# Kernel optimization log

Measured on AMD Instinct MI355X. Metric: run time of the kernel, lower is better.

Reference implementation:

```python
import jax, jax.numpy as jnp
import numpy as np

B, C, IMG, P, D, L, NH, DFF = 8, 2, 256, 16, 1024, 8, 16, 4096
HP = IMG // P          # 16 patches per side
N = HP * HP            # 256 patch tokens
S = N + 1              # + cls token
HD = D // NH           # 64 head dim


def _ln(x, w, b, eps=1e-5):
    mu = x.mean(-1, keepdims=True)
    var = ((x - mu) ** 2).mean(-1, keepdims=True)
    return (x - mu) * jax.lax.rsqrt(var + eps) * w + b


def _decay_mask():
    # RetNetRelPos2d(D, NH, initial_value=1, heads_range=NH): per-head log-decay
    decay = jnp.log(1.0 - 2.0 ** (-1.0 - NH * jnp.arange(NH, dtype=jnp.float32) / NH))
    idx = jnp.arange(HP)
    gy, gx = jnp.meshgrid(idx, idx, indexing='ij')
    grid = jnp.stack([gy.ravel(), gx.ravel()], -1)                 # [N,2]
    dist = jnp.abs(grid[:, None] - grid[None, :]).sum(-1)          # [N,N] Manhattan
    mask = decay[:, None, None] * dist.astype(jnp.float32)        # [NH,N,N]
    return jnp.pad(mask, ((0, 0), (1, 0), (1, 0)))                 # cls: zero decay


def setup_inputs() -> dict:
    key = jax.random.key(0)
    ks = iter(jax.random.split(key, 16))
    g = lambda shape: jax.random.normal(next(ks), shape, jnp.float32) * 0.02
    return dict(
        imgs=jax.random.normal(next(ks), (B, C, IMG, IMG), jnp.float32),
        patch_w=g((C, P, P, D)), patch_b=jnp.zeros((D,), jnp.float32),
        cls_tok=g((1, 1, D)),
        ln1_w=jnp.ones((L, D), jnp.float32), ln1_b=jnp.zeros((L, D), jnp.float32),
        wq=g((L, D, D)), wk=g((L, D, D)), wv=g((L, D, D)),
        bq=jnp.zeros((L, D), jnp.float32), bk=jnp.zeros((L, D), jnp.float32), bv=jnp.zeros((L, D), jnp.float32),
        wo=g((L, D, D)), bo=jnp.zeros((L, D), jnp.float32),
        ln2_w=jnp.ones((L, D), jnp.float32), ln2_b=jnp.zeros((L, D), jnp.float32),
        w1=g((L, D, DFF)), b1=jnp.zeros((L, DFF), jnp.float32),
        w2=g((L, DFF, D)), b2=jnp.zeros((L, D), jnp.float32),
        normf_w=jnp.ones((D,), jnp.float32), normf_b=jnp.zeros((D,), jnp.float32),
        enpred_w=g((D, P * P * 2)), enpred_b=jnp.zeros((P * P * 2,), jnp.float32),
    )


def reference(imgs, patch_w, patch_b, cls_tok, ln1_w, ln1_b, wq, wk, wv, bq, bk, bv,
              wo, bo, ln2_w, ln2_b, w1, b1, w2, b2, normf_w, normf_b, enpred_w, enpred_b):
    b = imgs.shape[0]
    # PatchEmbed: conv with stride==kernel == patch extraction + linear
    xp = imgs.reshape(b, C, HP, P, HP, P)
    x = jnp.einsum('nchpwq,cpqd->nhwd', xp, patch_w).reshape(b, N, D) + patch_b
    residual = x
    x = jnp.concatenate([jnp.broadcast_to(cls_tok, (b, 1, D)), x], axis=1)  # [b,S,D]
    mask = _decay_mask()  # [NH,S,S]
    scale = HD ** -0.5
    for i in range(L):  # RMT blocks: pre-LN MaSA (softmax(qk*scale + decay)) + pre-LN GELU MLP
        h = _ln(x, ln1_w[i], ln1_b[i])
        q = (h @ wq[i] + bq[i]).reshape(b, S, NH, HD)
        k = (h @ wk[i] + bk[i]).reshape(b, S, NH, HD)
        v = (h @ wv[i] + bv[i]).reshape(b, S, NH, HD)
        logits = jnp.einsum('bqhd,bkhd->bhqk', q, k) * scale + mask
        attn = jax.nn.softmax(logits, axis=-1)
        o = jnp.einsum('bhqk,bkhd->bqhd', attn, v).reshape(b, S, D)
        x = x + o @ wo[i] + bo[i]
        h = _ln(x, ln2_w[i], ln2_b[i])
        x = x + jax.nn.gelu(h @ w1[i] + b1[i], approximate=False) @ w2[i] + b2[i]
    x = _ln(x, normf_w, normf_b)
    # PGSA on patch tokens as [b,D,HP,HP]
    t = x[:, 1:, :].transpose(0, 2, 1).reshape(b, D, HP, HP)
    n = HP * HP - 1
    mu = t.mean(axis=(2, 3), keepdims=True)
    xm2 = (t - mu) ** 2
    y = xm2 / (4.0 * (xm2.sum(axis=(2, 3), keepdims=True) / n + 1e-4)) + 0.5
    t = t * jax.nn.sigmoid(y)
    tokens = t.reshape(b, D, N).transpose(0, 2, 1) + residual
    pred = tokens @ enpred_w + enpred_b  # [b,N,P*P*2]
    # unpatchify -> [b,2,IMG,IMG]
    u = pred.reshape(b, HP, HP, P, P, 2)
    return jnp.einsum('nhwpqc->nchpwq', u).reshape(b, 2, IMG, IMG)
```

## Files before the change

kernel.cpp:

```cpp
#include <hip/hip_runtime.h>
#include <cstdint>
#include <cstddef>

#define BB    8
#define CCH   2
#define IMGD  256
#define PDIM  16
#define DD    1024
#define LLAY  8
#define NHEAD 16
#define DFFD  4096
#define NTOK  256
#define SD    257
#define HDD   64
#define MTOK  (BB*SD)
#define MPAT  (BB*NTOK)
#define MPAD  2176
#define KPAD  288
#define QSTR  3072

typedef unsigned short u16;
typedef __bf16 bf16x8 __attribute__((ext_vector_type(8)));
typedef float  f32x4  __attribute__((ext_vector_type(4)));

__device__ __forceinline__ u16 f2bf(float f) {
    uint32_t u = __float_as_uint(f);
    u += 0x7FFF + ((u >> 16) & 1);
    return (u16)(u >> 16);
}
__device__ __forceinline__ int imin(int a, int b) { return a < b ? a : b; }

#define GLB(p)  ((const __attribute__((address_space(1))) void*)(uintptr_t)(p))
#define LDSP(p) ((__attribute__((address_space(3))) void*)(uint32_t)(uintptr_t)(p))

__device__ __forceinline__ void tp64(const float* __restrict__ W,
                                     u16* __restrict__ WT, int K, int N,
                                     int k0, int n0, float (*t)[65])
{
    const int c = threadIdx.x & 63, r4 = threadIdx.x >> 6;
    #pragma unroll
    for (int i = 0; i < 16; ++i) {
        const int r = i * 4 + r4;
        t[r][c] = W[(size_t)(k0 + r) * N + n0 + c];
    }
    __syncthreads();
    #pragma unroll
    for (int i = 0; i < 16; ++i) {
        const int r = i * 4 + r4;
        WT[(size_t)(n0 + r) * K + k0 + c] = f2bf(t[c][r]);
    }
}

__device__ __forceinline__ void tp_dispatch(
    int t, const float* wqN, const float* wkN, const float* wvN,
    const float* woN, const float* w1N, const float* w2N,
    u16* WTqkvN, u16* WTwoN, u16* WTw1N, u16* WTw2N, float (*tb)[65])
{
    if (t < 768) {
        const int which = t >> 8, local = t & 255;
        const float* W = which == 0 ? wqN : which == 1 ? wkN : wvN;
        tp64(W, WTqkvN + (size_t)which * 1024 * DD, DD, DD,
             (local >> 4) * 64, (local & 15) * 64, tb);
    } else if (t < 1024) {
        const int local = t - 768;
        tp64(woN, WTwoN, DD, DD, (local >> 4) * 64, (local & 15) * 64, tb);
    } else if (t < 2048) {
        const int local = t - 1024;
        tp64(w1N, WTw1N, DD, DFFD, (local >> 6) * 64, (local & 63) * 64, tb);
    } else {
        const int local = t - 2048;
        tp64(w2N, WTw2N, DFFD, DD, (local >> 4) * 64, (local & 15) * 64, tb);
    }
}

__global__ __launch_bounds__(256) void mlp1_tp(
    const u16* __restrict__ A, const u16* __restrict__ BT,
    const float* __restrict__ bias, u16* __restrict__ Cout, int M,
    const float* __restrict__ wqN, const float* __restrict__ wkN,
    const float* __restrict__ wvN, const float* __restrict__ woN,
    const float* __restrict__ w1N, const float* __restrict__ w2N,
    u16* __restrict__ WTqkvN, u16* __restrict__ WTwoN,
    u16* __restrict__ WTw1N, u16* __restrict__ WTw2N)
{
    __shared__ float smem[64 * 65];
    if (blockIdx.y >= 17) {
        const int t = (blockIdx.y - 17) * 32 + blockIdx.x;
        tp_dispatch(t, wqN, wkN, wvN, woN, w1N, w2N,
                    WTqkvN, WTwoN, WTw1N, WTw2N, (float(*)[65])smem);
        return;
    }
    u16* lds = (u16*)smem;
    const int N = DFFD, K = DD;
    const int tid = threadIdx.x, wid = tid >> 6, lane = tid & 63;
    const int m0 = blockIdx.y * 128, n0 = blockIdx.x * 128;
    const int wm = (wid >> 1) * 64, wn = (wid & 1) * 64;
    const int srow = lane >> 2, scol = (lane & 3) * 8;
    const int l15 = lane & 15, loct = lane >> 4;

    f32x4 acc[4][4] = {};
    const size_t arow = (size_t)(m0 + wid * 16 + srow) * K + scol;
    const size_t brow = (size_t)(n0 + wid * 16 + srow) * K + scol;
    u16* ldsA = lds + wid * 512;
    u16* ldsB = lds + 4096 + wid * 512;

    for (int k0 = 0; k0 < K; k0 += 32) {
        __builtin_amdgcn_global_load_lds(GLB(A  + arow + k0),                 LDSP(ldsA),        16, 0, 0);
        __builtin_amdgcn_global_load_lds(GLB(A  + arow + (size_t)64*K + k0),  LDSP(ldsA + 2048), 16, 0, 0);
        __builtin_amdgcn_global_load_lds(GLB(BT + brow + k0),                 LDSP(ldsB),        16, 0, 0);
        __builtin_amdgcn_global_load_lds(GLB(BT + brow + (size_t)64*K + k0),  LDSP(ldsB + 2048), 16, 0, 0);
        __syncthreads();
        bf16x8 af[4], bfr[4];
        #pragma unroll
        for (int i = 0; i < 4; ++i)
            af[i] = *(const bf16x8*)(lds + (wm + i * 16 + l15) * 32 + loct * 8);
        #pragma unroll
        for (int j = 0; j < 4; ++j)
            bfr[j] = *(const bf16x8*)(lds + 4096 + (wn + j * 16 + l15) * 32 + loct * 8);
        #pragma unroll
        for (int i = 0; i < 4; ++i)
            #pragma unroll
            for (int j = 0; j < 4; ++j)
                acc[i][j] = __builtin_amdgcn_mfma_f32_16x16x32_bf16(af[i], bfr[j], acc[i][j], 0, 0, 0);
        __syncthreads();
    }

    #pragma unroll
    for (int j = 0; j < 4; ++j) {
        const int col = n0 + wn + j * 16 + l15;
        const float bv = bias[col];
        #pragma unroll
        for (int i = 0; i < 4; ++i) {
            const int rbase = m0 + wm + i * 16 + loct * 4;
            #pragma unroll
            for (int r = 0; r < 4; ++r) {
                const int row = rbase + r;
                if (row < M) {
                    float v = acc[i][j][r] + bv;
                    v = 0.5f * v * (1.f + erff(v * 0.70710678118654752f));
                    Cout[(size_t)row * N + col] = f2bf(v);
                }
            }
        }
    }
}

template<int SPLIT>
__global__ __launch_bounds__(256) void gemm128_skp(
    const u16* __restrict__ A, const u16* __restrict__ BT,
    float* __restrict__ P, int M, int N, int K)
{
    __shared__ u16 lds[8192];
    const int tid = threadIdx.x, wid = tid >> 6, lane = tid & 63;
    const int m0 = blockIdx.y * 128, n0 = blockIdx.x * 128;
    const int wm = (wid >> 1) * 64, wn = (wid & 1) * 64;
    const int srow = lane >> 2, scol = (lane & 3) * 8;
    const int l15 = lane & 15, loct = lane >> 4;
    const int Ks = K / SPLIT;
    const int kb = blockIdx.z * Ks;

    f32x4 acc[4][4] = {};
    const size_t arow = (size_t)(m0 + wid * 16 + srow) * K + scol + kb;
    const size_t brow = (size_t)(n0 + wid * 16 + srow) * K + scol + kb;
    u16* ldsA = lds + wid * 512;
    u16* ldsB = lds + 4096 + wid * 512;

    for (int k0 = 0; k0 < Ks; k0 += 32) {
        __builtin_amdgcn_global_load_lds(GLB(A  + arow + k0),                 LDSP(ldsA),        16, 0, 0);
        __builtin_amdgcn_global_load_lds(GLB(A  + arow + (size_t)64*K + k0),  LDSP(ldsA + 2048), 16, 0, 0);
        __builtin_amdgcn_global_load_lds(GLB(BT + brow + k0),                 LDSP(ldsB),        16, 0, 0);
        __builtin_amdgcn_global_load_lds(GLB(BT + brow + (size_t)64*K + k0),  LDSP(ldsB + 2048), 16, 0, 0);
        __syncthreads();
        bf16x8 af[4], bfr[4];
        #pragma unroll
        for (int i = 0; i < 4; ++i)
            af[i] = *(const bf16x8*)(lds + (wm + i * 16 + l15) * 32 + loct * 8);
        #pragma unroll
        for (int j = 0; j < 4; ++j)
            bfr[j] = *(const bf16x8*)(lds + 4096 + (wn + j * 16 + l15) * 32 + loct * 8);
        #pragma unroll
        for (int i = 0; i < 4; ++i)
            #pragma unroll
            for (int j = 0; j < 4; ++j)
                acc[i][j] = __builtin_amdgcn_mfma_f32_16x16x32_bf16(af[i], bfr[j], acc[i][j], 0, 0, 0);
        __syncthreads();
    }

    float* Pz = P + (size_t)blockIdx.z * M * N;
    #pragma unroll
    for (int j = 0; j < 4; ++j) {
        const int col = n0 + wn + j * 16 + l15;
        #pragma unroll
        for (int i = 0; i < 4; ++i) {
            const int rbase = m0 + wm + i * 16 + loct * 4;
            #pragma unroll
            for (int r = 0; r < 4; ++r) {
                const int row = rbase + r;
                if (row < M) Pz[(size_t)row * N + col] = acc[i][j][r];
            }
        }
    }
}

__global__ __launch_bounds__(256) void gemm_qkv(
    const u16* __restrict__ A, const u16* __restrict__ BT,
    const float* __restrict__ bq, const float* __restrict__ bk,
    const float* __restrict__ bvp,
    u16* __restrict__ QKVb, int M, int K)
{
    __shared__ u16 lds[8192];
    const int tid = threadIdx.x, wid = tid >> 6, lane = tid & 63;
    const int m0 = blockIdx.y * 128, n0 = blockIdx.x * 128;
    const int wm = (wid >> 1) * 64, wn = (wid & 1) * 64;
    const int srow = lane >> 2, scol = (lane & 3) * 8;
    const int l15 = lane & 15, loct = lane >> 4;

    f32x4 acc[4][4] = {};
    const size_t arow = (size_t)(m0 + wid * 16 + srow) * K + scol;
    const size_t brow = (size_t)(n0 + wid * 16 + srow) * K + scol;
    u16* ldsA = lds + wid * 512;
    u16* ldsB = lds + 4096 + wid * 512;

    for (int k0 = 0; k0 < K; k0 += 32) {
        __builtin_amdgcn_global_load_lds(GLB(A  + arow + k0),                 LDSP(ldsA),        16, 0, 0);
        __builtin_amdgcn_global_load_lds(GLB(A  + arow + (size_t)64*K + k0),  LDSP(ldsA + 2048), 16, 0, 0);
        __builtin_amdgcn_global_load_lds(GLB(BT + brow + k0),                 LDSP(ldsB),        16, 0, 0);
        __builtin_amdgcn_global_load_lds(GLB(BT + brow + (size_t)64*K + k0),  LDSP(ldsB + 2048), 16, 0, 0);
        __syncthreads();
        bf16x8 af[4], bfr[4];
        #pragma unroll
        for (int i = 0; i < 4; ++i)
            af[i] = *(const bf16x8*)(lds + (wm + i * 16 + l15) * 32 + loct * 8);
        #pragma unroll
        for (int j = 0; j < 4; ++j)
            bfr[j] = *(const bf16x8*)(lds + 4096 + (wn + j * 16 + l15) * 32 + loct * 8);
        #pragma unroll
        for (int i = 0; i < 4; ++i)
            #pragma unroll
            for (int j = 0; j < 4; ++j)
                acc[i][j] = __builtin_amdgcn_mfma_f32_16x16x32_bf16(af[i], bfr[j], acc[i][j], 0, 0, 0);
        __syncthreads();
    }

    #pragma unroll
    for (int j = 0; j < 4; ++j) {
        const int col = n0 + wn + j * 16 + l15;
        const float bval = (col < 1024) ? bq[col]
                         : (col < 2048) ? bk[col - 1024]
                                        : bvp[col - 2048];
        #pragma unroll
        for (int i = 0; i < 4; ++i) {
            const int rbase = m0 + wm + i * 16 + loct * 4;
            #pragma unroll
            for (int r = 0; r < 4; ++r) {
                const int row = rbase + r;
                if (row < M)
                    QKVb[(size_t)row * QSTR + col] = f2bf(acc[i][j][r] + bval);
            }
        }
    }
}

__global__ __launch_bounds__(256) void vt_k(const u16* __restrict__ QKVb,
                                            u16* __restrict__ VTg)
{
    __shared__ u16 t[64][66];
    const int h0 = blockIdx.x * 64, k0 = blockIdx.y * 64, b = blockIdx.z;
    const int c = threadIdx.x & 63, r4 = threadIdx.x >> 6;
    #pragma unroll
    for (int i = 0; i < 16; ++i) {
        const int key = k0 + i * 4 + r4;
        t[i * 4 + r4][c] = (key < SD)
            ? QKVb[((size_t)(b * SD + key)) * QSTR + 2048 + h0 + c] : (u16)0;
    }
    __syncthreads();
    const int key = k0 + c;
    if (key < KPAD) {
        #pragma unroll
        for (int i = 0; i < 16; ++i) {
            const int hd = i * 4 + r4;
            VTg[((size_t)(b * 1024 + h0 + hd)) * KPAD + key] = t[c][hd];
        }
    }
}

__global__ __launch_bounds__(256) void patch_tp(
    const u16* __restrict__ A, const u16* __restrict__ BT,
    const float* __restrict__ bias, float* __restrict__ Cout,
    const float* __restrict__ wq0, const float* __restrict__ wk0,
    const float* __restrict__ wv0, const float* __restrict__ wo0,
    const float* __restrict__ w10, const float* __restrict__ w20,
    u16* __restrict__ WTqkv0, u16* __restrict__ WTwo0,
    u16* __restrict__ WTw10, u16* __restrict__ WTw20)
{
    __shared__ float smem[64 * 65];
    if (blockIdx.y >= 32) {
        const int t = (blockIdx.y - 32) * 16 + blockIdx.x;
        tp_dispatch(t, wq0, wk0, wv0, wo0, w10, w20,
                    WTqkv0, WTwo0, WTw10, WTw20, (float(*)[65])smem);
        return;
    }
    u16* lds = (u16*)smem;
    const int N = DD, K = 512;
    const int tid = threadIdx.x, wid = tid >> 6, lane = tid & 63;
    const int m0 = blockIdx.y * 64, n0 = blockIdx.x * 64;
    const int wm = (wid >> 1) * 32, wn = (wid & 1) * 32;
    const int srow = lane >> 2, scol = (lane & 3) * 8;
    const int l15 = lane & 15, loct = lane >> 4;

    f32x4 acc[2][2] = {};
    const size_t arow = (size_t)(m0 + wid * 16 + srow) * K + scol;
    const size_t brow = (size_t)(n0 + wid * 16 + srow) * K + scol;
    u16* ldsA = lds + wid * 512;
    u16* ldsB = lds + 4096 + wid * 512;

    for (int k0 = 0; k0 < K; k0 += 64) {
        __builtin_amdgcn_global_load_lds(GLB(A  + arow + k0),      LDSP(ldsA),        16, 0, 0);
        __builtin_amdgcn_global_load_lds(GLB(A  + arow + k0 + 32), LDSP(ldsA + 2048), 16, 0, 0);
        __builtin_amdgcn_global_load_lds(GLB(BT + brow + k0),      LDSP(ldsB),        16, 0, 0);
        __builtin_amdgcn_global_load_lds(GLB(BT + brow + k0 + 32), LDSP(ldsB + 2048), 16, 0, 0);
        __syncthreads();
        #pragma unroll
        for (int t = 0; t < 2; ++t) {
            bf16x8 af[2], bfr[2];
            #pragma unroll
            for (int i = 0; i < 2; ++i)
                af[i] = *(const bf16x8*)(lds + t * 2048 + (wm + i * 16 + l15) * 32 + loct * 8);
            #pragma unroll
            for (int j = 0; j < 2; ++j)
                bfr[j] = *(const bf16x8*)(lds + 4096 + t * 2048 + (wn + j * 16 + l15) * 32 + loct * 8);
            #pragma unroll
            for (int i = 0; i < 2; ++i)
                #pragma unroll
                for (int j = 0; j < 2; ++j)
                    acc[i][j] = __builtin_amdgcn_mfma_f32_16x16x32_bf16(af[i], bfr[j], acc[i][j], 0, 0, 0);
        }
        __syncthreads();
    }

    #pragma unroll
    for (int j = 0; j < 2; ++j) {
        const int col = n0 + wn + j * 16 + l15;
        const float bv = bias[col];
        #pragma unroll
        for (int i = 0; i < 2; ++i) {
            const int rbase = m0 + wm + i * 16 + loct * 4;
            #pragma unroll
            for (int r = 0; r < 4; ++r) {
                const int row = rbase + r;
                Cout[(size_t)row * N + col] = acc[i][j][r] + bv;
            }
        }
    }
}

template<int ACT, int OBF>
__global__ __launch_bounds__(256) void gemm64(
    const u16* __restrict__ A, const u16* __restrict__ BT,
    const float* __restrict__ bias, const float* __restrict__ Cin,
    void* __restrict__ Cout, int M, int N, int K)
{
    __shared__ u16 lds[8192];
    const int tid = threadIdx.x, wid = tid >> 6, lane = tid & 63;
    const int m0 = blockIdx.y * 64, n0 = blockIdx.x * 64;
    const int wm = (wid >> 1) * 32, wn = (wid & 1) * 32;
    const int srow = lane >> 2, scol = (lane & 3) * 8;
    const int l15 = lane & 15, loct = lane >> 4;

    f32x4 acc[2][2] = {};
    const size_t arow = (size_t)(m0 + wid * 16 + srow) * K + scol;
    const size_t brow = (size_t)(n0 + wid * 16 + srow) * K + scol;
    u16* ldsA = lds + wid * 512;
    u16* ldsB = lds + 4096 + wid * 512;

    for (int k0 = 0; k0 < K; k0 += 64) {
        __builtin_amdgcn_global_load_lds(GLB(A  + arow + k0),      LDSP(ldsA),        16, 0, 0);
        __builtin_amdgcn_global_load_lds(GLB(A  + arow + k0 + 32), LDSP(ldsA + 2048), 16, 0, 0);
        __builtin_amdgcn_global_load_lds(GLB(BT + brow + k0),      LDSP(ldsB),        16, 0, 0);
        __builtin_amdgcn_global_load_lds(GLB(BT + brow + k0 + 32), LDSP(ldsB + 2048), 16, 0, 0);
        __syncthreads();
        #pragma unroll
        for (int t = 0; t < 2; ++t) {
            bf16x8 af[2], bfr[2];
            #pragma unroll
            for (int i = 0; i < 2; ++i)
                af[i] = *(const bf16x8*)(lds + t * 2048 + (wm + i * 16 + l15) * 32 + loct * 8);
            #pragma unroll
            for (int j = 0; j < 2; ++j)
                bfr[j] = *(const bf16x8*)(lds + 4096 + t * 2048 + (wn + j * 16 + l15) * 32 + loct * 8);
            #pragma unroll
            for (int i = 0; i < 2; ++i)
                #pragma unroll
                for (int j = 0; j < 2; ++j)
                    acc[i][j] = __builtin_amdgcn_mfma_f32_16x16x32_bf16(af[i], bfr[j], acc[i][j], 0, 0, 0);
        }
        __syncthreads();
    }

    #pragma unroll
    for (int j = 0; j < 2; ++j) {
        const int col = n0 + wn + j * 16 + l15;
        const float bv = bias[col];
        #pragma unroll
        for (int i = 0; i < 2; ++i) {
            const int rbase = m0 + wm + i * 16 + loct * 4;
            #pragma unroll
            for (int r = 0; r < 4; ++r) {
                const int row = rbase + r;
                if (row < M) {
                    float v = acc[i][j][r] + bv;
                    if (ACT) v = 0.5f * v * (1.f + erff(v * 0.70710678118654752f));
                    if (Cin) v += Cin[(size_t)row * N + col];
                    if (OBF) ((u16*)Cout)[(size_t)row * N + col] = f2bf(v);
                    else     ((float*)Cout)[(size_t)row * N + col] = v;
                }
            }
        }
    }
}

__global__ __launch_bounds__(256) void attn_fused(
    const u16* __restrict__ QKVb, const u16* __restrict__ VTg,
    u16* __restrict__ O)
{
    __shared__ u16 P[4][16][296];
    const int tid = threadIdx.x, wid = tid >> 6, lane = tid & 63;
    const int l15 = lane & 15, loct = lane >> 4;
    const int bh = blockIdx.x, b = bh >> 4, h = bh & 15;
    const int q0 = blockIdx.y * 64 + wid * 16;

    const size_t qkbase = (size_t)b * SD * QSTR + h * 64;
    const u16* qp = QKVb + qkbase + (size_t)imin(q0 + l15, SD - 1) * QSTR;
    const bf16x8 qf0 = *(const bf16x8*)(qp + loct * 8);
    const bf16x8 qf1 = *(const bf16x8*)(qp + 32 + loct * 8);

    f32x4 s[17];
    #pragma unroll
    for (int nt = 0; nt < 17; ++nt) {
        const u16* kp = QKVb + qkbase + (size_t)imin(nt * 16 + l15, SD - 1) * QSTR + 1024;
        const bf16x8 kf0 = *(const bf16x8*)(kp + loct * 8);
        const bf16x8 kf1 = *(const bf16x8*)(kp + 32 + loct * 8);
        f32x4 a = {};
        a = __builtin_amdgcn_mfma_f32_16x16x32_bf16(qf0, kf0, a, 0, 0, 0);
        a = __builtin_amdgcn_mfma_f32_16x16x32_bf16(qf1, kf1, a, 0, 0, 0);
        s[nt] = a;
    }

    const float dec = logf(1.f - exp2f(-1.f - (float)h));
    const int qb = q0 + loct * 4;
    float rmax[4] = {-3.4e38f, -3.4e38f, -3.4e38f, -3.4e38f};
    #pragma unroll
    for (int nt = 0; nt < 17; ++nt) {
        const int key = nt * 16 + l15;
        #pragma unroll
        for (int r = 0; r < 4; ++r) {
            float v;
            if (key >= SD) {
                v = -1e30f;
            } else {
                v = s[nt][r] * 0.125f;
                const int q = qb + r;
                if (q > 0 && key > 0) {
                    const int nq = q - 1, nk = key - 1;
                    const int dist = abs((nq >> 4) - (nk >> 4)) + abs((nq & 15) - (nk & 15));
                    v += dec * (float)dist;
                }
            }
            s[nt][r] = v;
            rmax[r] = fmaxf(rmax[r], v);
        }
    }
    #pragma unroll
    for (int r = 0; r < 4; ++r) {
        #pragma unroll
        for (int m = 1; m < 16; m <<= 1) rmax[r] = fmaxf(rmax[r], __shfl_xor(rmax[r], m));
    }
    float rsum[4] = {0.f, 0.f, 0.f, 0.f};
    #pragma unroll
    for (int nt = 0; nt < 17; ++nt)
        #pragma unroll
        for (int r = 0; r < 4; ++r) {
            const float e = __expf(s[nt][r] - rmax[r]);
            s[nt][r] = e;
            rsum[r] += e;
        }
    #pragma unroll
    for (int r = 0; r < 4; ++r) {
        #pragma unroll
        for (int m = 1; m < 16; m <<= 1) rsum[r] += __shfl_xor(rsum[r], m);
        rsum[r] = 1.f / rsum[r];
    }
    #pragma unroll
    for (int nt = 0; nt < 17; ++nt)
        #pragma unroll
        for (int r = 0; r < 4; ++r)
            P[wid][loct * 4 + r][nt * 16 + l15] = f2bf(s[nt][r] * rsum[r]);
    {
        const int rr = lane >> 2, cc = (lane & 3) * 4;
        #pragma unroll
        for (int i = 0; i < 4; ++i) P[wid][rr][272 + cc + i] = 0;
    }

    f32x4 o[4] = {};
    const u16* vrow = VTg + ((size_t)b * 1024 + h * 64) * KPAD;
    #pragma unroll
    for (int ks = 0; ks < 9; ++ks) {
        const bf16x8 pf = *(const bf16x8*)&P[wid][l15][ks * 32 + loct * 8];
        #pragma unroll
        for (int j = 0; j < 4; ++j) {
            const bf16x8 vf = *(const bf16x8*)(vrow + (size_t)(j * 16 + l15) * KPAD + ks * 32 + loct * 8);
            o[j] = __builtin_amdgcn_mfma_f32_16x16x32_bf16(pf, vf, o[j], 0, 0, 0);
        }
    }
    #pragma unroll
    for (int j = 0; j < 4; ++j)
        #pragma unroll
        for (int r = 0; r < 4; ++r) {
            const int q = qb + r;
            if (q < SD) O[((size_t)(b * SD + q)) * DD + h * 64 + j * 16 + l15] = f2bf(o[j][r]);
        }
}

__global__ __launch_bounds__(256) void transpose_bf16_b(
    const float* __restrict__ W, u16* __restrict__ WT, int K, int N,
    size_t sstrideZ, size_t dstrideZ)
{
    __shared__ float t[64][65];
    tp64(W + (size_t)blockIdx.z * sstrideZ, WT + (size_t)blockIdx.z * dstrideZ,
         K, N, blockIdx.y * 64, blockIdx.x * 64, t);
}

__global__ __launch_bounds__(256) void im2col_k(const float* __restrict__ imgs,
                                                u16* __restrict__ Ao)
{
    const int idx = blockIdx.x * 256 + threadIdx.x;
    const int k = idx & 511, m = idx >> 9;
    const int b = m >> 8, n = m & 255;
    const int hp = n >> 4, wp = n & 15;
    const int c = k >> 8, p = (k >> 4) & 15, q = k & 15;
    Ao[idx] = f2bf(imgs[(((size_t)b * CCH + c) * IMGD + hp * PDIM + p) * IMGD + wp * PDIM + q]);
}

__global__ __launch_bounds__(256) void build_x_k(const float* __restrict__ RES,
                                                 const float* __restrict__ cls,
                                                 float* __restrict__ X)
{
    const int idx = blockIdx.x * 256 + threadIdx.x;
    const int d = idx & 1023;
    const int r = idx >> 10;
    const int b = r / SD;
    const int s = r - b * SD;
    X[idx] = (s == 0) ? cls[d] : RES[((size_t)(b * NTOK + s - 1)) * DD + d];
}

template<int NP, int OBF>
__global__ __launch_bounds__(256) void ln_rows_c(
    float* __restrict__ X, const float* __restrict__ PB, size_t pstride,
    const float* __restrict__ badd,
    const float* __restrict__ w, const float* __restrict__ bsrc,
    void* __restrict__ Y)
{
    const int wid = threadIdx.x >> 6, lane = threadIdx.x & 63;
    const int row = blockIdx.x * 4 + wid;
    float* xr = X + (size_t)row * DD;
    float4 v[4];
    float s = 0.f, s2 = 0.f;
    #pragma unroll
    for (int i = 0; i < 4; ++i) {
        const int cc = (i * 64 + lane) * 4;
        v[i] = *(const float4*)(xr + cc);
        if (NP) {
            const float4 bb = *(const float4*)(badd + cc);
            v[i].x += bb.x; v[i].y += bb.y; v[i].z += bb.z; v[i].w += bb.w;
            #pragma unroll
            for (int p = 0; p < NP; ++p) {
                const float4 pv = *(const float4*)(PB + (size_t)p * pstride + (size_t)row * DD + cc);
                v[i].x += pv.x; v[i].y += pv.y; v[i].z += pv.z; v[i].w += pv.w;
            }
            *(float4*)(xr + cc) = v[i];
        }
        s  += v[i].x + v[i].y + v[i].z + v[i].w;
        s2 += v[i].x * v[i].x + v[i].y * v[i].y + v[i].z * v[i].z + v[i].w * v[i].w;
    }
    #pragma unroll
    for (int off = 1; off < 64; off <<= 1) {
        s  += __shfl_xor(s, off);
        s2 += __shfl_xor(s2, off);
    }
    const float mu  = s * (1.f / 1024.f);
    const float var = fmaf(-mu, mu, s2 * (1.f / 1024.f));
    const float ri  = rsqrtf(var + 1e-5f);
    #pragma unroll
    for (int i = 0; i < 4; ++i) {
        const int cc = (i * 64 + lane) * 4;
        const float4 wv = *(const float4*)(w + cc);
        const float4 bv = *(const float4*)(bsrc + cc);
        float4 o;
        o.x = (v[i].x - mu) * ri * wv.x + bv.x;
        o.y = (v[i].y - mu) * ri * wv.y + bv.y;
        o.z = (v[i].z - mu) * ri * wv.z + bv.z;
        o.w = (v[i].w - mu) * ri * wv.w + bv.w;
        if (OBF) {
            ushort4 o4 = make_ushort4(f2bf(o.x), f2bf(o.y), f2bf(o.z), f2bf(o.w));
            *(ushort4*)((u16*)Y + (size_t)row * DD + cc) = o4;
        } else {
            *(float4*)((float*)Y + (size_t)row * DD + cc) = o;
        }
    }
}

__global__ __launch_bounds__(256) void pgsa_k(const float* __restrict__ Xf,
                                              const float* __restrict__ RES,
                                              u16* __restrict__ TOK)
{
    const int bd = blockIdx.x;
    const int b = bd >> 10, dch = bd & 1023;
    const int n = threadIdx.x;
    const float t = Xf[((size_t)(b * SD + 1 + n)) * DD + dch];
    __shared__ float red[4];
    float s = t;
    #pragma unroll
    for (int off = 1; off < 64; off <<= 1) s += __shfl_xor(s, off);
    if ((n & 63) == 0) red[n >> 6] = s;
    __syncthreads();
    const float mu = (red[0] + red[1] + red[2] + red[3]) * (1.f / 256.f);
    const float xm = t - mu;
    const float xm2 = xm * xm;
    __syncthreads();
    float s2 = xm2;
    #pragma unroll
    for (int off = 1; off < 64; off <<= 1) s2 += __shfl_xor(s2, off);
    if ((n & 63) == 0) red[n >> 6] = s2;
    __syncthreads();
    const float tot2 = red[0] + red[1] + red[2] + red[3];
    const float y = xm2 / (4.f * (tot2 * (1.f / 255.f) + 1e-4f)) + 0.5f;
    const float sig = 1.f / (1.f + expf(-y));
    const size_t ri = ((size_t)b * NTOK + n) * DD + dch;
    TOK[ri] = f2bf(fmaf(t, sig, RES[ri]));
}

__global__ __launch_bounds__(256) void unpatch_k(const float* __restrict__ PRED,
                                                 float* __restrict__ out)
{
    const int idx = blockIdx.x * 256 + threadIdx.x;
    const int j = idx & 255, i = (idx >> 8) & 255;
    const int c = (idx >> 16) & 1, b = idx >> 17;
    const int hp = i >> 4, p = i & 15, wp = j >> 4, q = j & 15;
    out[idx] = PRED[((size_t)b * NTOK + hp * 16 + wp) * 512 + (p * 16 + q) * 2 + c];
}

extern "C" void kernel_launch(void* const* d_in, const int* in_sizes, int n_in,
                              void* d_out, int out_size, void* d_ws, size_t ws_size,
                              hipStream_t stream)
{
    const float* imgs     = (const float*)d_in[0];
    const float* patch_w  = (const float*)d_in[1];
    const float* patch_b  = (const float*)d_in[2];
    const float* cls_tok  = (const float*)d_in[3];
    const float* ln1_w    = (const float*)d_in[4];
    const float* ln1_b    = (const float*)d_in[5];
    const float* wq       = (const float*)d_in[6];
    const float* wk       = (const float*)d_in[7];
    const float* wv       = (const float*)d_in[8];
    const float* bq       = (const float*)d_in[9];
    const float* bk       = (const float*)d_in[10];
    const float* bv       = (const float*)d_in[11];
    const float* wo       = (const float*)d_in[12];
    const float* bo       = (const float*)d_in[13];
    const float* ln2_w    = (const float*)d_in[14];
    const float* ln2_b    = (const float*)d_in[15];
    const float* w1       = (const float*)d_in[16];
    const float* b1       = (const float*)d_in[17];
    const float* w2       = (const float*)d_in[18];
    const float* b2       = (const float*)d_in[19];
    const float* normf_w  = (const float*)d_in[20];
    const float* normf_b  = (const float*)d_in[21];
    const float* enpred_w = (const float*)d_in[22];
    const float* enpred_b = (const float*)d_in[23];
    float* out = (float*)d_out;

    char* w = (char*)d_ws;
    float* X     = (float*)w;            w += (size_t)MTOK * DD * 4;
    float* RES   = (float*)w;            w += (size_t)MPAT * DD * 4;
    u16*   QKVb  = (u16*)w;              w += (size_t)MPAD * QSTR * 2;
    u16*   VTg   = (u16*)w;              w += (size_t)BB * 1024 * KPAD * 2;
    char*  UNION = w;                    w += (size_t)MPAD * DFFD * 2;
    u16*   Hb    = (u16*)w;              w += (size_t)MPAD * DD * 2;
    u16*   Ob    = (u16*)w;              w += (size_t)MPAD * DD * 2;
    float* PART  = (float*)w;            w += (size_t)4 * MTOK * DD * 4;
    u16*   WTqkv = (u16*)w;              w += (size_t)LLAY * 3072 * DD * 2;
    u16*   WTwo  = (u16*)w;              w += (size_t)LLAY * DD * DD * 2;
    u16*   WTw1  = (u16*)w;              w += (size_t)LLAY * DFFD * DD * 2;
    u16*   WTw2  = (u16*)w;              w += (size_t)LLAY * DD * DFFD * 2;
    u16*   WTpe  = (u16*)w;              w += (size_t)DD * 512 * 2;
    u16*   WTen  = (u16*)w;              w += (size_t)512 * DD * 2;

    u16*   IM2b  = (u16*)UNION;
    u16*   GELUb = (u16*)UNION;
    float* PRED  = (float*)UNION;
    float* Hf    = (float*)QKVb;
    u16*   TOKb  = Hb;
    const size_t PSTR = (size_t)MTOK * DD;

    hipLaunchKernelGGL(transpose_bf16_b, dim3(DD / 64, 512 / 64, 1), dim3(256), 0, stream,
                       patch_w, WTpe, 512, DD, (size_t)0, (size_t)0);
    hipLaunchKernelGGL(transpose_bf16_b, dim3(512 / 64, DD / 64, 1), dim3(256), 0, stream,
                       enpred_w, WTen, DD, 512, (size_t)0, (size_t)0);
    hipLaunchKernelGGL(im2col_k, dim3(4096), dim3(256), 0, stream, imgs, IM2b);

    hipLaunchKernelGGL(patch_tp, dim3(DD / 64, 32 + 192), dim3(256), 0, stream,
                       IM2b, WTpe, patch_b, RES,
                       wq, wk, wv, wo, w1, w2,
                       WTqkv, WTwo, WTw1, WTw2);
    hipLaunchKernelGGL(build_x_k, dim3(MTOK * DD / 256), dim3(256), 0, stream, RES, cls_tok, X);

    for (int i = 0; i < LLAY; ++i) {
        if (i == 0)
            hipLaunchKernelGGL((ln_rows_c<0,1>), dim3(MTOK / 4), dim3(256), 0, stream,
                               X, (const float*)nullptr, (size_t)0, (const float*)nullptr,
                               ln1_w + i * DD, ln1_b + i * DD, (void*)Hb);
        else
            hipLaunchKernelGGL((ln_rows_c<4,1>), dim3(MTOK / 4), dim3(256), 0, stream,
                               X, PART, PSTR, b2 + (i - 1) * DD,
                               ln1_w + i * DD, ln1_b + i * DD, (void*)Hb);
        hipLaunchKernelGGL(gemm_qkv, dim3(3072 / 128, 17), dim3(256), 0, stream,
                           Hb, WTqkv + (size_t)i * 3072 * DD,
                           bq + i * DD, bk + i * DD, bv + i * DD, QKVb, MTOK, DD);
        hipLaunchKernelGGL(vt_k, dim3(16, 5, BB), dim3(256), 0, stream, QKVb, VTg);
        hipLaunchKernelGGL(attn_fused, dim3(BB * NHEAD, 5), dim3(256), 0, stream,
                           QKVb, VTg, Ob);
        hipLaunchKernelGGL((gemm64<0,0>), dim3(DD / 64, 33), dim3(256), 0, stream,
                           Ob, WTwo + (size_t)i * DD * DD, bo + i * DD, X, (void*)X, MTOK, DD, DD);
        hipLaunchKernelGGL((ln_rows_c<0,1>), dim3(MTOK / 4), dim3(256), 0, stream,
                           X, (const float*)nullptr, (size_t)0, (const float*)nullptr,
                           ln2_w + i * DD, ln2_b + i * DD, (void*)Hb);
        if (i < LLAY - 1) {
            const size_t n1 = (size_t)(i + 1);
            hipLaunchKernelGGL(mlp1_tp, dim3(DFFD / 128, 17 + 96), dim3(256), 0, stream,
                               Hb, WTw1 + (size_t)i * DFFD * DD, b1 + i * DFFD, GELUb, MTOK,
                               wq + n1 * DD * DD, wk + n1 * DD * DD, wv + n1 * DD * DD,
                               wo + n1 * DD * DD, w1 + n1 * DD * DFFD, w2 + n1 * DFFD * DD,
                               WTqkv + n1 * 3072 * DD, WTwo + n1 * DD * DD,
                               WTw1 + n1 * DFFD * DD, WTw2 + n1 * DD * DFFD);
        } else {
            hipLaunchKernelGGL(mlp1_tp, dim3(DFFD / 128, 17), dim3(256), 0, stream,
                               Hb, WTw1 + (size_t)i * DFFD * DD, b1 + i * DFFD, GELUb, MTOK,
                               (const float*)nullptr, (const float*)nullptr, (const float*)nullptr,
                               (const float*)nullptr, (const float*)nullptr, (const float*)nullptr,
                               (u16*)nullptr, (u16*)nullptr, (u16*)nullptr, (u16*)nullptr);
        }
        hipLaunchKernelGGL((gemm128_skp<4>), dim3(DD / 128, 17, 4), dim3(256), 0, stream,
                           GELUb, WTw2 + (size_t)i * DD * DFFD, PART, MTOK, DD, DFFD);
    }

    hipLaunchKernelGGL((ln_rows_c<4,0>), dim3(MTOK / 4), dim3(256), 0, stream,
                       X, PART, PSTR, b2 + (LLAY - 1) * DD, normf_w, normf_b, (void*)Hf);
    hipLaunchKernelGGL(pgsa_k, dim3(BB * DD), dim3(256), 0, stream, Hf, RES, TOKb);
    hipLaunchKernelGGL((gemm64<0,0>), dim3(512 / 64, MPAT / 64), dim3(256), 0, stream,
                       TOKb, WTen, enpred_b, (const float*)nullptr, (void*)PRED, MPAT, 512, DD);
    hipLaunchKernelGGL(unpatch_k, dim3(4096), dim3(256), 0, stream, PRED, out);
}
```

Baseline: 1.925 ms.

## Fuse V transpose into QKV GEMM epilogue, restructure PGSA and unpatchify

The QKV GEMM now writes Q and K into a narrower 2048-column buffer and scatters V directly into the transposed VTg layout through LDS. This removes the separate vt_k kernel and its round trip through global memory, and VTg is zeroed once with a memset so the key padding stays valid. PGSA switches to coalesced per-channel column processing that computes sum and sum of squares in one pass, and unpatchify reads float2 pairs and writes both channels. The scattered, strided VTg writes in the epilogue may be poorly coalesced, and the one-pass variance formula changes numerics slightly.

Result: faster. 1.858 ms (-3.5%).

```diff
diff --git a/kernel.cpp b/kernel.cpp
--- a/kernel.cpp
+++ b/kernel.cpp
@@ -17,7 +17,6 @@
 #define MPAT  (BB*NTOK)
 #define MPAD  2176
 #define KPAD  288
-#define QSTR  3072
 
 typedef unsigned short u16;
 typedef __bf16 bf16x8 __attribute__((ext_vector_type(8)));
@@ -205,9 +204,9 @@
     const u16* __restrict__ A, const u16* __restrict__ BT,
     const float* __restrict__ bq, const float* __restrict__ bk,
     const float* __restrict__ bvp,
-    u16* __restrict__ QKVb, int M, int K)
-{
-    __shared__ u16 lds[8192];
+    u16* __restrict__ QKb, u16* __restrict__ VTg, int M, int K)
+{
+    __shared__ u16 lds[128 * 66];
     const int tid = threadIdx.x, wid = tid >> 6, lane = tid & 63;
     const int m0 = blockIdx.y * 128, n0 = blockIdx.x * 128;
     const int wm = (wid >> 1) * 64, wn = (wid & 1) * 64;
@@ -241,44 +240,57 @@
         __syncthreads();
     }
 
-    #pragma unroll
-    for (int j = 0; j < 4; ++j) {
-        const int col = n0 + wn + j * 16 + l15;
-        const float bval = (col < 1024) ? bq[col]
-                         : (col < 2048) ? bk[col - 1024]
-                                        : bvp[col - 2048];
-        #pragma unroll
-        for (int i = 0; i < 4; ++i) {
-            const int rbase = m0 + wm + i * 16 + loct * 4;
-            #pragma unroll
-            for (int r = 0; r < 4; ++r) {
-                const int row = rbase + r;
-                if (row < M)
-                    QKVb[(size_t)row * QSTR + col] = f2bf(acc[i][j][r] + bval);
-            }
-        }
-    }
-}
-
-__global__ __launch_bounds__(256) void vt_k(const u16* __restrict__ QKVb,
-                                            u16* __restrict__ VTg)
-{
-    __shared__ u16 t[64][66];
-    const int h0 = blockIdx.x * 64, k0 = blockIdx.y * 64, b = blockIdx.z;
-    const int c = threadIdx.x & 63, r4 = threadIdx.x >> 6;
-    #pragma unroll
-    for (int i = 0; i < 16; ++i) {
-        const int key = k0 + i * 4 + r4;
-        t[i * 4 + r4][c] = (key < SD)
-            ? QKVb[((size_t)(b * SD + key)) * QSTR + 2048 + h0 + c] : (u16)0;
-    }
-    __syncthreads();
-    const int key = k0 + c;
-    if (key < KPAD) {
-        #pragma unroll
-        for (int i = 0; i < 16; ++i) {
-            const int hd = i * 4 + r4;
-            VTg[((size_t)(b * 1024 + h0 + hd)) * KPAD + key] = t[c][hd];
+    if (n0 < 2048) {
+        #pragma unroll
+        for (int j = 0; j < 4; ++j) {
+            const int col = n0 + wn + j * 16 + l15;
+            const float bval = (col < 1024) ? bq[col] : bk[col - 1024];
+            #pragma unroll
+            for (int i = 0; i < 4; ++i) {
+                const int rbase = m0 + wm + i * 16 + loct * 4;
+                #pragma unroll
+                for (int r = 0; r < 4; ++r) {
+                    const int row = rbase + r;
+                    if (row < M)
+                        QKb[(size_t)row * 2048 + col] = f2bf(acc[i][j][r] + bval);
+                }
+            }
+        }
+    } else {
+        const int hd0 = n0 - 2048;
+        #pragma unroll
+        for (int h = 0; h < 2; ++h) {
+            __syncthreads();
+            if ((wn >> 6) == h) {
+                #pragma unroll
+                for (int j = 0; j < 4; ++j) {
+                    const int c = j * 16 + l15;
+                    const float bval = bvp[hd0 + h * 64 + c];
+                    #pragma unroll
+                    for (int i = 0; i < 4; ++i) {
+                        const int rbase = wm + i * 16 + loct * 4;
+                        #pragma unroll
+                        for (int r = 0; r < 4; ++r)
+                            lds[(rbase + r) * 66 + c] = f2bf(acc[i][j][r] + bval);
+                    }
+                }
+            }
+            __syncthreads();
+            const int rowLane = tid & 63, cIdx = tid >> 6;
+            #pragma unroll
+            for (int cc = 0; cc < 16; ++cc) {
+                const int c = cIdx * 16 + cc;
+                #pragma unroll
+                for (int rh = 0; rh < 2; ++rh) {
+                    const int row = rowLane + rh * 64;
+                    const int g = m0 + row;
+                    if (g < M) {
+                        const int b = g / SD, key = g - b * SD;
+                        VTg[((size_t)b * 1024 + hd0 + h * 64 + c) * KPAD + key] =
+                            lds[row * 66 + c];
+                    }
+                }
+            }
         }
     }
 }
@@ -419,7 +431,7 @@
 }
 
 __global__ __launch_bounds__(256) void attn_fused(
-    const u16* __restrict__ QKVb, const u16* __restrict__ VTg,
+    const u16* __restrict__ QKb, const u16* __restrict__ VTg,
     u16* __restrict__ O)
 {
     __shared__ u16 P[4][16][296];
@@ -428,15 +440,15 @@
     const int bh = blockIdx.x, b = bh >> 4, h = bh & 15;
     const int q0 = blockIdx.y * 64 + wid * 16;
 
-    const size_t qkbase = (size_t)b * SD * QSTR + h * 64;
-    const u16* qp = QKVb + qkbase + (size_t)imin(q0 + l15, SD - 1) * QSTR;
+    const size_t qkbase = (size_t)b * SD * 2048 + h * 64;
+    const u16* qp = QKb + qkbase + (size_t)imin(q0 + l15, SD - 1) * 2048;
     const bf16x8 qf0 = *(const bf16x8*)(qp + loct * 8);
     const bf16x8 qf1 = *(const bf16x8*)(qp + 32 + loct * 8);
 
     f32x4 s[17];
     #pragma unroll
     for (int nt = 0; nt < 17; ++nt) {
-        const u16* kp = QKVb + qkbase + (size_t)imin(nt * 16 + l15, SD - 1) * QSTR + 1024;
+        const u16* kp = QKb + qkbase + (size_t)imin(nt * 16 + l15, SD - 1) * 2048 + 1024;
         const bf16x8 kf0 = *(const bf16x8*)(kp + loct * 8);
         const bf16x8 kf1 = *(const bf16x8*)(kp + 32 + loct * 8);
         f32x4 a = {};
@@ -612,40 +624,51 @@
                                               const float* __restrict__ RES,
                                               u16* __restrict__ TOK)
 {
-    const int bd = blockIdx.x;
-    const int b = bd >> 10, dch = bd & 1023;
-    const int n = threadIdx.x;
-    const float t = Xf[((size_t)(b * SD + 1 + n)) * DD + dch];
-    __shared__ float red[4];
-    float s = t;
-    #pragma unroll
-    for (int off = 1; off < 64; off <<= 1) s += __shfl_xor(s, off);
-    if ((n & 63) == 0) red[n >> 6] = s;
+    const int b = blockIdx.y, ch = blockIdx.x * 32 + (threadIdx.x & 31);
+    const int r8 = threadIdx.x >> 5;
+    float v[32];
+    float s = 0.f, s2 = 0.f;
+    #pragma unroll
+    for (int it = 0; it < 32; ++it) {
+        const int tok = it * 8 + r8;
+        v[it] = Xf[((size_t)(b * SD + 1 + tok)) * DD + ch];
+        s += v[it];
+        s2 = fmaf(v[it], v[it], s2);
+    }
+    __shared__ float rs[8][32], rs2[8][32];
+    rs[r8][threadIdx.x & 31] = s;
+    rs2[r8][threadIdx.x & 31] = s2;
     __syncthreads();
-    const float mu = (red[0] + red[1] + red[2] + red[3]) * (1.f / 256.f);
-    const float xm = t - mu;
-    const float xm2 = xm * xm;
-    __syncthreads();
-    float s2 = xm2;
-    #pragma unroll
-    for (int off = 1; off < 64; off <<= 1) s2 += __shfl_xor(s2, off);
-    if ((n & 63) == 0) red[n >> 6] = s2;
-    __syncthreads();
-    const float tot2 = red[0] + red[1] + red[2] + red[3];
-    const float y = xm2 / (4.f * (tot2 * (1.f / 255.f) + 1e-4f)) + 0.5f;
-    const float sig = 1.f / (1.f + expf(-y));
-    const size_t ri = ((size_t)b * NTOK + n) * DD + dch;
-    TOK[ri] = f2bf(fmaf(t, sig, RES[ri]));
+    s = 0.f; s2 = 0.f;
+    #pragma unroll
+    for (int k = 0; k < 8; ++k) {
+        s += rs[k][threadIdx.x & 31];
+        s2 += rs2[k][threadIdx.x & 31];
+    }
+    const float mu = s * (1.f / 256.f);
+    const float tot2 = fmaf(-mu, s, s2);
+    const float dinv = 1.f / (4.f * (tot2 * (1.f / 255.f) + 1e-4f));
+    #pragma unroll
+    for (int it = 0; it < 32; ++it) {
+        const int tok = it * 8 + r8;
+        const float xm = v[it] - mu;
+        const float y = fmaf(xm * xm, dinv, 0.5f);
+        const float sig = 1.f / (1.f + expf(-y));
+        const size_t ri = ((size_t)b * NTOK + tok) * DD + ch;
+        TOK[ri] = f2bf(fmaf(v[it], sig, RES[ri]));
+    }
 }
 
 __global__ __launch_bounds__(256) void unpatch_k(const float* __restrict__ PRED,
                                                  float* __restrict__ out)
 {
     const int idx = blockIdx.x * 256 + threadIdx.x;
-    const int j = idx & 255, i = (idx >> 8) & 255;
-    const int c = (idx >> 16) & 1, b = idx >> 17;
+    const int j = idx & 255, i = (idx >> 8) & 255, b = idx >> 16;
     const int hp = i >> 4, p = i & 15, wp = j >> 4, q = j & 15;
-    out[idx] = PRED[((size_t)b * NTOK + hp * 16 + wp) * 512 + (p * 16 + q) * 2 + c];
+    const float2 f2 = *(const float2*)&PRED[(((size_t)b * NTOK + hp * 16 + wp) * 512) + (p * 16 + q) * 2];
+    const size_t o0 = (size_t)b * 131072 + (size_t)i * 256 + j;
+    out[o0]         = f2.x;
+    out[o0 + 65536] = f2.y;
 }
 
 extern "C" void kernel_launch(void* const* d_in, const int* in_sizes, int n_in,
@@ -681,7 +704,7 @@
     char* w = (char*)d_ws;
     float* X     = (float*)w;            w += (size_t)MTOK * DD * 4;
     float* RES   = (float*)w;            w += (size_t)MPAT * DD * 4;
-    u16*   QKVb  = (u16*)w;              w += (size_t)MPAD * QSTR * 2;
+    u16*   QKb   = (u16*)w;              w += (size_t)MPAD * 2048 * 2;
     u16*   VTg   = (u16*)w;              w += (size_t)BB * 1024 * KPAD * 2;
     char*  UNION = w;                    w += (size_t)MPAD * DFFD * 2;
     u16*   Hb    = (u16*)w;              w += (size_t)MPAD * DD * 2;
@@ -697,9 +720,11 @@
     u16*   IM2b  = (u16*)UNION;
     u16*   GELUb = (u16*)UNION;
     float* PRED  = (float*)UNION;
-    float* Hf    = (float*)QKVb;
+    float* Hf    = (float*)QKb;
     u16*   TOKb  = Hb;
     const size_t PSTR = (size_t)MTOK * DD;
+
+    hipMemsetAsync(VTg, 0, (size_t)BB * 1024 * KPAD * 2, stream);
 
     hipLaunchKernelGGL(transpose_bf16_b, dim3(DD / 64, 512 / 64, 1), dim3(256), 0, stream,
                        patch_w, WTpe, 512, DD, (size_t)0, (size_t)0);
@@ -724,10 +749,9 @@
                                ln1_w + i * DD, ln1_b + i * DD, (void*)Hb);
         hipLaunchKernelGGL(gemm_qkv, dim3(3072 / 128, 17), dim3(256), 0, stream,
                            Hb, WTqkv + (size_t)i * 3072 * DD,
-                           bq + i * DD, bk + i * DD, bv + i * DD, QKVb, MTOK, DD);
-        hipLaunchKernelGGL(vt_k, dim3(16, 5, BB), dim3(256), 0, stream, QKVb, VTg);
+                           bq + i * DD, bk + i * DD, bv + i * DD, QKb, VTg, MTOK, DD);
         hipLaunchKernelGGL(attn_fused, dim3(BB * NHEAD, 5), dim3(256), 0, stream,
-                           QKVb, VTg, Ob);
+                           QKb, VTg, Ob);
         hipLaunchKernelGGL((gemm64<0,0>), dim3(DD / 64, 33), dim3(256), 0, stream,
                            Ob, WTwo + (size_t)i * DD * DD, bo + i * DD, X, (void*)X, MTOK, DD, DD);
         hipLaunchKernelGGL((ln_rows_c<0,1>), dim3(MTOK / 4), dim3(256), 0, stream,
@@ -754,8 +778,8 @@
 
     hipLaunchKernelGGL((ln_rows_c<4,0>), dim3(MTOK / 4), dim3(256), 0, stream,
                        X, PART, PSTR, b2 + (LLAY - 1) * DD, normf_w, normf_b, (void*)Hf);
-    hipLaunchKernelGGL(pgsa_k, dim3(BB * DD), dim3(256), 0, stream, Hf, RES, TOKb);
+    hipLaunchKernelGGL(pgsa_k, dim3(32, BB), dim3(256), 0, stream, Hf, RES, TOKb);
     hipLaunchKernelGGL((gemm64<0,0>), dim3(512 / 64, MPAT / 64), dim3(256), 0, stream,
                        TOKb, WTen, enpred_b, (const float*)nullptr, (void*)PRED, MPAT, 512, DD);
-    hipLaunchKernelGGL(unpatch_k, dim3(4096), dim3(256), 0, stream, PRED, out);
-}
+    hipLaunchKernelGGL(unpatch_k, dim3(2048), dim3(256), 0, stream, PRED, out);
+}
```
